# Kernel tuning notes

Measured on AMD Instinct MI355X. Metric: run time of the kernel, lower is better.

Reference implementation:

```python
import jax, jax.numpy as jnp
import numpy as np

B, D, K, P = 512, 2048, 128, 5

def setup_inputs() -> dict:
    key = jax.random.key(0)
    k1, k2 = jax.random.split(key)
    x = jax.random.normal(k1, (B, D), dtype=jnp.float32)
    theta = 0.05 * jax.random.normal(k2, (D, K, P), dtype=jnp.float32)
    log_weight_scale = jnp.zeros((K, P), dtype=jnp.float32)
    bias = -jnp.ones((K,), dtype=jnp.float32)  # layer inits bias to -1
    return {"x": x, "theta": theta, "log_weight_scale": log_weight_scale, "bias": bias}

def reference(x, theta, log_weight_scale, bias):
    b = x.shape[0]
    # weight-normalized kernel: [D, K, P]
    norm = jnp.sqrt(jnp.sum(theta * theta, axis=0))            # [K, P]
    kernel = theta * (jnp.exp(log_weight_scale) / norm)[None]  # [D, K, P]
    actv = jnp.einsum('bd,dkp->bkp', x, kernel)                # [B, K, P]
    # pairwise L1 over P: [B, K, B]
    diff = jnp.abs(actv[:, :, :, None] - jnp.transpose(actv, (1, 2, 0))[None])  # [B,K,P,B]
    abs_dif = jnp.sum(diff, axis=2) + 1e6 * jnp.eye(b, dtype=x.dtype)[:, None, :]
    f = jnp.sum(jnp.exp(-abs_dif), axis=2) + bias[None, :]     # [B, K]
    return jnp.concatenate([x, f], axis=1)                     # [B, D+K]
```

## Files before the change

### kernel.cpp

```cpp
#include <hip/hip_runtime.h>
#include <math.h>

#define BSZ 512
#define DD 2048
#define KK 128
#define PP 5
#define NCOL (KK * PP)
#define OUTW (DD + KK)
#define LOG2E 1.4426950408889634f

#define KSPLIT 16
#define GK (DD / KSPLIT)

typedef __attribute__((ext_vector_type(8))) short bf16x8;
typedef __attribute__((ext_vector_type(4))) float f32x4;

#define WS_NORM 0
#define WS_ACTV (WS_NORM + NCOL)
#define WS_XB (WS_ACTV + BSZ * NCOL)
#define WS_THT (WS_XB + BSZ * DD / 2)
#define WS_PART (WS_THT + NCOL * DD / 2)

__device__ inline ushort f2b(float f) {
    unsigned u = __float_as_uint(f);
    u += 0x7FFF + ((u >> 16) & 1);
    return (ushort)(u >> 16);
}

#define SWZ(r, c) ((((r) * 128) + ((c) ^ (((r) & 7) << 3))))

__global__ __launch_bounds__(256) void prep_kernel(const float* __restrict__ theta,
                                                   const float* __restrict__ x,
                                                   float* __restrict__ norm,
                                                   ushort* __restrict__ thT,
                                                   ushort* __restrict__ xb) {
    __shared__ float partial[32][8];
    __shared__ ushort sT[64][68];

    const int bid = blockIdx.x;
    const int t   = threadIdx.x;

    if (bid < 80) {
        const int c8  = bid * 8;
        const int col = c8 + (t & 7);
        const int g   = t >> 3;
        const float* p = theta + (size_t)g * NCOL + col;
        float s = 0.f;
#pragma unroll
        for (int j = 0; j < 64; ++j) {
            float v = p[(size_t)j * 32 * NCOL];
            s += v * v;
        }
        partial[g][t & 7] = s;
        __syncthreads();
        if (t < 8) {
            float acc = 0.f;
#pragma unroll
            for (int gg = 0; gg < 32; ++gg) acc += partial[gg][t];
            norm[c8 + t] = acc;
        }
    } else if (bid < 400) {
        const int tb    = bid - 80;
        const int kz    = (tb & 31) * 64;
        const int nz    = (tb >> 5) * 64;
        const int c4    = t & 15;
        const int rbase = t >> 4;
#pragma unroll
        for (int i = 0; i < 4; ++i) {
            int r = rbase + i * 16;
            float4 v = *(const float4*)&theta[(size_t)(kz + r) * NCOL + nz + c4 * 4];
            sT[c4 * 4 + 0][r] = f2b(v.x);
            sT[c4 * 4 + 1][r] = f2b(v.y);
            sT[c4 * 4 + 2][r] = f2b(v.z);
            sT[c4 * 4 + 3][r] = f2b(v.w);
        }
        __syncthreads();
#pragma unroll
        for (int i = 0; i < 2; ++i) {
            int slot = t + i * 256;
            int rr   = slot >> 3;
            int cc   = (slot & 7) * 8;
            ushort4 w0 = *(const ushort4*)&sT[rr][cc];
            ushort4 w1 = *(const ushort4*)&sT[rr][cc + 4];
            ushort* dst = &thT[(size_t)(nz + rr) * DD + kz + cc];
            *(ushort4*)&dst[0] = w0;
            *(ushort4*)&dst[4] = w1;
        }
    } else {
        const int b2 = bid - 400;
#pragma unroll
        for (int i = 0; i < 4; ++i) {
            int base = b2 * 4096 + i * 1024 + t * 4;
            float4 v = *(const float4*)&x[base];
            ushort4 w;
            w.x = f2b(v.x); w.y = f2b(v.y); w.z = f2b(v.z); w.w = f2b(v.w);
            *(ushort4*)&xb[base] = w;
        }
    }
}

__global__ __launch_bounds__(256) void gemm_kernel(const ushort* __restrict__ xb,
                                                   const ushort* __restrict__ thT,
                                                   ushort* __restrict__ parth,
                                                   const float* __restrict__ x,
                                                   float* __restrict__ out) {
    __shared__ ushort lA[64 * 128];
    __shared__ ushort lB[64 * 128];

    const int bx = blockIdx.x;
    if (bx >= 1280) {
        const int bid = bx - 1280;
        for (int i = bid * 256 + threadIdx.x; i < BSZ * (DD / 4); i += 80 * 256) {
            int r = i >> 9;
            int c = i & 511;
            float4 v = *(const float4*)&x[(size_t)r * DD + c * 4];
            *(float4*)&out[(size_t)r * OUTW + c * 4] = v;
        }
        return;
    }

    const int t    = threadIdx.x;
    const int lane = t & 63;
    const int wave = t >> 6;
    const int mt8  = bx & 7;
    const int rest = bx >> 3;
    const int bn   = (rest % 10) * 64;
    const int bm   = mt8 * 64;
    const int z    = rest / 10;
    const int kz   = z * GK;

    const ushort* gA = xb  + (size_t)bm * DD + kz;
    const ushort* gB = thT + (size_t)bn * DD + kz;

    const int srr = t >> 4;
    const int sss = t & 15;

    uint4 va[4], vb[4];
#pragma unroll
    for (int i = 0; i < 4; ++i) {
        int rr = srr + i * 16;
        va[i] = *(const uint4*)&gA[(size_t)rr * DD + sss * 8];
        vb[i] = *(const uint4*)&gB[(size_t)rr * DD + sss * 8];
    }
#pragma unroll
    for (int i = 0; i < 4; ++i) {
        int rr = srr + i * 16;
        *(uint4*)&lA[SWZ(rr, sss * 8)] = va[i];
        *(uint4*)&lB[SWZ(rr, sss * 8)] = vb[i];
    }
    __syncthreads();

    const int fr = lane & 15;
    const int g  = lane >> 4;
    const int mr = (wave >> 1) * 32 + fr;
    const int nr = (wave & 1) * 32 + fr;

    f32x4 acc[2][2] = {};
#pragma unroll
    for (int ks = 0; ks < 4; ++ks) {
        const int kc = ks * 32 + g * 8;
        bf16x8 a0 = *(const bf16x8*)&lA[SWZ(mr,      kc)];
        bf16x8 a1 = *(const bf16x8*)&lA[SWZ(mr + 16, kc)];
        bf16x8 b0 = *(const bf16x8*)&lB[SWZ(nr,      kc)];
        bf16x8 b1 = *(const bf16x8*)&lB[SWZ(nr + 16, kc)];
        acc[0][0] = __builtin_amdgcn_mfma_f32_16x16x32_bf16(a0, b0, acc[0][0], 0, 0, 0);
        acc[0][1] = __builtin_amdgcn_mfma_f32_16x16x32_bf16(a0, b1, acc[0][1], 0, 0, 0);
        acc[1][0] = __builtin_amdgcn_mfma_f32_16x16x32_bf16(a1, b0, acc[1][0], 0, 0, 0);
        acc[1][1] = __builtin_amdgcn_mfma_f32_16x16x32_bf16(a1, b1, acc[1][1], 0, 0, 0);
    }

    ushort* base = parth + (size_t)z * (BSZ * NCOL);
#pragma unroll
    for (int mt = 0; mt < 2; ++mt)
#pragma unroll
        for (int nt = 0; nt < 2; ++nt) {
            int row = bm + (wave >> 1) * 32 + mt * 16 + g * 4;
            int col = bn + (wave & 1) * 32 + nt * 16 + fr;
            ushort* dst = base + (size_t)row * NCOL + col;
#pragma unroll
            for (int reg = 0; reg < 4; ++reg)
                dst[(size_t)reg * NCOL] = f2b(acc[mt][nt][reg]);
        }
}

__global__ __launch_bounds__(256) void reduce_kernel(const ushort* __restrict__ parth,
                                                     const float* __restrict__ norm,
                                                     const float* __restrict__ lws,
                                                     float* __restrict__ actv) {
    int i   = (blockIdx.x * 256 + threadIdx.x) * 2;
    int b   = i / NCOL;
    int col = i - b * NCOL;
    float s0 = 0.f, s1 = 0.f;
#pragma unroll
    for (int q = 0; q < KSPLIT; ++q) {
        unsigned u = *(const unsigned*)&parth[(size_t)q * (BSZ * NCOL) + i];
        s0 += __uint_as_float(u << 16);
        s1 += __uint_as_float(u & 0xffff0000u);
    }
    const float sc0 = __builtin_amdgcn_exp2f(lws[col] * LOG2E) *
                      __builtin_amdgcn_rsqf(norm[col]) * LOG2E;
    const float sc1 = __builtin_amdgcn_exp2f(lws[col + 1] * LOG2E) *
                      __builtin_amdgcn_rsqf(norm[col + 1]) * LOG2E;
    int k0 = col / 5,       p0 = col - k0 * 5;
    int k1 = (col + 1) / 5, p1 = (col + 1) - k1 * 5;
    actv[((size_t)k0 * BSZ + b) * PP + p0] = s0 * sc0;
    actv[((size_t)k1 * BSZ + b) * PP + p1] = s1 * sc1;
}

__global__ __launch_bounds__(256) void pairwise_kernel(const float* __restrict__ actv,
                                                       const float* __restrict__ bias,
                                                       float* __restrict__ out) {
    const int k   = blockIdx.x;
    const int bc  = blockIdx.y;
    const int tid = threadIdx.x;
    const int r   = tid & 63;
    const int seg = tid >> 6;

    __shared__ float sB[512][8];
    __shared__ float red[4][64];

    const float* col = actv + (size_t)k * (BSZ * PP);

    for (int i = tid; i < BSZ * PP; i += 256) {
        int rr = i / 5;
        sB[rr][i - rr * 5] = col[i];
    }

    const int b = bc * 64 + r;
    const float a0 = col[b * 5 + 0];
    const float a1 = col[b * 5 + 1];
    const float a2 = col[b * 5 + 2];
    const float a3 = col[b * 5 + 3];
    const float a4 = col[b * 5 + 4];
    __syncthreads();

    float acc0 = 0.f, acc1 = 0.f;
    const int j0 = seg * 128;
#pragma unroll 8
    for (int jj = 0; jj < 128; jj += 2) {
        const float4 v  = *(const float4*)&sB[j0 + jj][0];
        const float  v4 = sB[j0 + jj][4];
        float s = fabsf(a0 - v.x) + fabsf(a1 - v.y) + fabsf(a2 - v.z) +
                  fabsf(a3 - v.w) + fabsf(a4 - v4);
        acc0 += __builtin_amdgcn_exp2f(-s);
        const float4 w  = *(const float4*)&sB[j0 + jj + 1][0];
        const float  w4 = sB[j0 + jj + 1][4];
        float t = fabsf(a0 - w.x) + fabsf(a1 - w.y) + fabsf(a2 - w.z) +
                  fabsf(a3 - w.w) + fabsf(a4 - w4);
        acc1 += __builtin_amdgcn_exp2f(-t);
    }
    red[seg][r] = acc0 + acc1;
    __syncthreads();
    if (tid < 64) {
        float s = red[0][tid] + red[1][tid] + red[2][tid] + red[3][tid];
        out[(size_t)(bc * 64 + tid) * OUTW + DD + k] = s - 1.0f + bias[k];
    }
}

extern "C" void kernel_launch(void* const* d_in, const int* in_sizes, int n_in,
                              void* d_out, int out_size, void* d_ws, size_t ws_size,
                              hipStream_t stream) {
    const float* x     = (const float*)d_in[0];
    const float* theta = (const float*)d_in[1];
    const float* lws   = (const float*)d_in[2];
    const float* bias  = (const float*)d_in[3];
    float* out = (float*)d_out;

    float* ws     = (float*)d_ws;
    float* norm   = ws + WS_NORM;
    float* actv   = ws + WS_ACTV;
    ushort* xb    = (ushort*)(ws + WS_XB);
    ushort* thT   = (ushort*)(ws + WS_THT);
    ushort* parth = (ushort*)(ws + WS_PART);

    prep_kernel<<<656, 256, 0, stream>>>(theta, x, norm, thT, xb);
    gemm_kernel<<<1360, 256, 0, stream>>>(xb, thT, parth, x, out);
    reduce_kernel<<<640, 256, 0, stream>>>(parth, norm, lws, actv);
    pairwise_kernel<<<dim3(KK, 8), 256, 0, stream>>>(actv, bias, out);
}
```

Before: 102.1 us.

## Store actv row-major with coalesced stores and compute two rows per thread in pairwise

The reduce kernel now writes actv in its natural [B, K*P] layout with one float2 store per thread, instead of scattering each value into a [K, B, P] layout. The pairwise kernel gathers its column from that layout with a strided read. Each thread now handles two query rows against every shared-memory entry, so every LDS load is reused twice, and the grid is halved to 4 row chunks per k. This trades coalesced stores in reduce for strided loads in pairwise, and gives pairwise fewer blocks (512) and more registers per thread.

```diff
diff --git a/kernel.cpp b/kernel.cpp
--- a/kernel.cpp
+++ b/kernel.cpp
@@ -187,9 +187,7 @@
                                                      const float* __restrict__ norm,
                                                      const float* __restrict__ lws,
                                                      float* __restrict__ actv) {
-    int i   = (blockIdx.x * 256 + threadIdx.x) * 2;
-    int b   = i / NCOL;
-    int col = i - b * NCOL;
+    int i = (blockIdx.x * 256 + threadIdx.x) * 2;
     float s0 = 0.f, s1 = 0.f;
 #pragma unroll
     for (int q = 0; q < KSPLIT; ++q) {
@@ -197,63 +195,63 @@
         s0 += __uint_as_float(u << 16);
         s1 += __uint_as_float(u & 0xffff0000u);
     }
+    const int col = i % NCOL;
     const float sc0 = __builtin_amdgcn_exp2f(lws[col] * LOG2E) *
                       __builtin_amdgcn_rsqf(norm[col]) * LOG2E;
     const float sc1 = __builtin_amdgcn_exp2f(lws[col + 1] * LOG2E) *
                       __builtin_amdgcn_rsqf(norm[col + 1]) * LOG2E;
-    int k0 = col / 5,       p0 = col - k0 * 5;
-    int k1 = (col + 1) / 5, p1 = (col + 1) - k1 * 5;
-    actv[((size_t)k0 * BSZ + b) * PP + p0] = s0 * sc0;
-    actv[((size_t)k1 * BSZ + b) * PP + p1] = s1 * sc1;
+    float2 o = make_float2(s0 * sc0, s1 * sc1);
+    *(float2*)&actv[i] = o;
 }
 
 __global__ __launch_bounds__(256) void pairwise_kernel(const float* __restrict__ actv,
                                                        const float* __restrict__ bias,
                                                        float* __restrict__ out) {
-    const int k   = blockIdx.x;
-    const int bc  = blockIdx.y;
-    const int tid = threadIdx.x;
-    const int r   = tid & 63;
-    const int seg = tid >> 6;
+    const int k    = blockIdx.x;
+    const int rc   = blockIdx.y;
+    const int tid  = threadIdx.x;
+    const int lane = tid & 63;
+    const int seg  = tid >> 6;
 
     __shared__ float sB[512][8];
-    __shared__ float red[4][64];
-
-    const float* col = actv + (size_t)k * (BSZ * PP);
+    __shared__ float red[4][128];
 
     for (int i = tid; i < BSZ * PP; i += 256) {
         int rr = i / 5;
-        sB[rr][i - rr * 5] = col[i];
-    }
-
-    const int b = bc * 64 + r;
-    const float a0 = col[b * 5 + 0];
-    const float a1 = col[b * 5 + 1];
-    const float a2 = col[b * 5 + 2];
-    const float a3 = col[b * 5 + 3];
-    const float a4 = col[b * 5 + 4];
+        int p  = i - rr * 5;
+        sB[rr][p] = actv[(size_t)rr * NCOL + k * PP + p];
+    }
+
+    const int r0 = rc * 128 + lane;
+    const int r1 = r0 + 64;
+    float a0[PP], a1[PP];
+#pragma unroll
+    for (int p = 0; p < PP; ++p) {
+        a0[p] = actv[(size_t)r0 * NCOL + k * PP + p];
+        a1[p] = actv[(size_t)r1 * NCOL + k * PP + p];
+    }
     __syncthreads();
 
     float acc0 = 0.f, acc1 = 0.f;
     const int j0 = seg * 128;
-#pragma unroll 8
-    for (int jj = 0; jj < 128; jj += 2) {
+#pragma unroll 4
+    for (int jj = 0; jj < 128; ++jj) {
         const float4 v  = *(const float4*)&sB[j0 + jj][0];
         const float  v4 = sB[j0 + jj][4];
-        float s = fabsf(a0 - v.x) + fabsf(a1 - v.y) + fabsf(a2 - v.z) +
-                  fabsf(a3 - v.w) + fabsf(a4 - v4);
+        float s = fabsf(a0[0] - v.x) + fabsf(a0[1] - v.y) + fabsf(a0[2] - v.z) +
+                  fabsf(a0[3] - v.w) + fabsf(a0[4] - v4);
         acc0 += __builtin_amdgcn_exp2f(-s);
-        const float4 w  = *(const float4*)&sB[j0 + jj + 1][0];
-        const float  w4 = sB[j0 + jj + 1][4];
-        float t = fabsf(a0 - w.x) + fabsf(a1 - w.y) + fabsf(a2 - w.z) +
-                  fabsf(a3 - w.w) + fabsf(a4 - w4);
+        float t = fabsf(a1[0] - v.x) + fabsf(a1[1] - v.y) + fabsf(a1[2] - v.z) +
+                  fabsf(a1[3] - v.w) + fabsf(a1[4] - v4);
         acc1 += __builtin_amdgcn_exp2f(-t);
     }
-    red[seg][r] = acc0 + acc1;
+    red[seg][lane]      = acc0;
+    red[seg][lane + 64] = acc1;
     __syncthreads();
-    if (tid < 64) {
+
+    if (tid < 128) {
         float s = red[0][tid] + red[1][tid] + red[2][tid] + red[3][tid];
-        out[(size_t)(bc * 64 + tid) * OUTW + DD + k] = s - 1.0f + bias[k];
+        out[(size_t)(rc * 128 + tid) * OUTW + DD + k] = s - 1.0f + bias[k];
     }
 }
 
@@ -276,5 +274,5 @@
     prep_kernel<<<656, 256, 0, stream>>>(theta, x, norm, thT, xb);
     gemm_kernel<<<1360, 256, 0, stream>>>(xb, thT, parth, x, out);
     reduce_kernel<<<640, 256, 0, stream>>>(parth, norm, lws, actv);
-    pairwise_kernel<<<dim3(KK, 8), 256, 0, stream>>>(actv, bias, out);
-}
+    pairwise_kernel<<<dim3(KK, 4), 256, 0, stream>>>(actv, bias, out);
+}
```

New measurement: 100.7 us. No clear change (-1.3%).
